# Kernel tuning notes

Measured on AMD Instinct MI355X. Metric: run time of the kernel, lower is better.

Reference implementation:

```python
import jax, jax.numpy as jnp
import numpy as np

N = 40000      # nodes
E = 320000     # edges (avg degree 8)
F_IN = 128     # input channels
H = 4          # attention heads
C = 64         # per-head hidden channels (hidden_features_size entries)
HC = H * C     # 256, width after head concat
OUT = 64       # output classes
BN_EPS = 1e-5
NEG_SLOPE = 0.2


def setup_inputs() -> dict:
    key = jax.random.key(0)
    ks = jax.random.split(key, 16)
    s1 = 1.0 / np.sqrt(F_IN)
    s2 = 1.0 / np.sqrt(HC)
    return {
        "x": jax.random.normal(ks[0], (N, F_IN), jnp.float32),
        "edge_index": jax.random.randint(ks[1], (2, E), 0, N, dtype=jnp.int64),
        "W1": jax.random.normal(ks[2], (F_IN, HC), jnp.float32) * s1,
        "a1_src": jax.random.normal(ks[3], (H, C), jnp.float32) * s2,
        "a1_dst": jax.random.normal(ks[4], (H, C), jnp.float32) * s2,
        "b1": jnp.zeros((HC,), jnp.float32),
        # BatchNorm1d(256)
        "bn1_gamma": jnp.ones((HC,), jnp.float32),
        "bn1_beta": jnp.zeros((HC,), jnp.float32),
        "W2": jax.random.normal(ks[5], (HC, HC), jnp.float32) * s2,
        "a2_src": jax.random.normal(ks[6], (H, C), jnp.float32) * s2,
        "a2_dst": jax.random.normal(ks[7], (H, C), jnp.float32) * s2,
        "b2": jnp.zeros((HC,), jnp.float32),
        # final projection Linear(256 -> 64)
        "linW": jax.random.normal(ks[8], (HC, OUT), jnp.float32) * s2,
        "linb": jnp.zeros((OUT,), jnp.float32),
    }


def gat_conv(x, W, a_src, a_dst, bias, src, dst):
    """PyG GATConv (concat=True, add_self_loops=False, negative_slope=0.2)."""
    h = (x @ W).reshape(-1, H, C)                       # [N,H,C]
    e_src = jnp.einsum("nhc,hc->nh", h, a_src)          # [N,H]
    e_dst = jnp.einsum("nhc,hc->nh", h, a_dst)          # [N,H]
    # per-edge unnormalized attention, message src -> dst
    e = jax.nn.leaky_relu(e_src[src] + e_dst[dst], NEG_SLOPE)   # [E,H]
    # segment softmax over incoming edges of each dst node
    m = jax.ops.segment_max(e, dst, num_segments=N)             # [N,H]
    p = jnp.exp(e - jax.lax.stop_gradient(m)[dst])              # [E,H]
    denom = jax.ops.segment_sum(p, dst, num_segments=N)         # [N,H]
    alpha = p / (denom[dst] + 1e-16)                            # [E,H]
    # weighted scatter-sum aggregation
    out = jax.ops.segment_sum(h[src] * alpha[:, :, None], dst, num_segments=N)  # [N,H,C]
    return out.reshape(-1, HC) + bias


def batch_norm(x, gamma, beta):
    mean = jnp.mean(x, axis=0)
    var = jnp.mean(jnp.square(x - mean), axis=0)
    return (x - mean) * jax.lax.rsqrt(var + BN_EPS) * gamma + beta


def reference(x, edge_index, W1, a1_src, a1_dst, b1, bn1_gamma, bn1_beta,
              W2, a2_src, a2_dst, b2, linW, linb):
    src, dst = edge_index[0], edge_index[1]
    h1 = gat_conv(x, W1, a1_src, a1_dst, b1, src, dst)
    h1 = jax.nn.elu(batch_norm(h1, bn1_gamma, bn1_beta))
    # dropout is identity in eval mode
    h2 = gat_conv(h1, W2, a2_src, a2_dst, b2, src, dst)
    # JumpingKnowledge 'max': elementwise max over layer outputs
    jk = jnp.maximum(h1, h2)
    return jk @ linW + linb
```

## Files before the change

kernel.cpp:

```cpp
#include <hip/hip_runtime.h>
#include <math.h>

#define N_NODES 40000
#define N_EDGES 320000
#define F_IN 128
#define NHEAD 4
#define HC 256
#define NOUT 64
#define SLOTCAP 40

typedef __attribute__((ext_vector_type(8))) __bf16 bf16x8;
typedef __attribute__((ext_vector_type(4))) float f32x4;

static __device__ __forceinline__ unsigned short f2bf(float f) {
    union { float f; unsigned u; } v; v.f = f;
    unsigned r = v.u + 0x7FFFu + ((v.u >> 16) & 1u);
    return (unsigned short)(r >> 16);
}
static __device__ __forceinline__ float bf2f(unsigned short s) {
    union { unsigned u; float f; } v; v.u = ((unsigned)s) << 16;
    return v.f;
}

__global__ __launch_bounds__(256) void prep_kernel(const float* __restrict__ W1,
                                                   const float* __restrict__ W2,
                                                   const float* __restrict__ linW,
                                                   unsigned short* __restrict__ W1t,
                                                   unsigned short* __restrict__ W2t,
                                                   unsigned short* __restrict__ linWt,
                                                   int* __restrict__ zero_ints,
                                                   float* __restrict__ bnacc) {
    int b = blockIdx.x, tid = threadIdx.x;
    if (b < 128) {
        int t = b * 256 + tid;
        int k = t >> 8, n = t & 255;
        W1t[n * 128 + k] = f2bf(W1[t]);
    } else if (b < 384) {
        int t = (b - 128) * 256 + tid;
        int k = t >> 8, n = t & 255;
        W2t[n * 256 + k] = f2bf(W2[t]);
    } else if (b < 448) {
        int t = (b - 384) * 256 + tid;
        int k = t >> 6, n = t & 63;
        linWt[n * 256 + k] = f2bf(linW[t]);
    } else if (b < 488) {
        int i = (b - 448) * 1024 + tid * 4;
        if (i < 40004) *(int4*)(zero_ints + i) = make_int4(0, 0, 0, 0);
    } else {
        if (tid < 512) bnacc[tid] = 0.f;
    }
}

template <int AMODE, int SCATTER>
__global__ __launch_bounds__(256) void gemm_wide(const void* __restrict__ Aptr,
                                                 const unsigned short* __restrict__ Bt,
                                                 const float* __restrict__ sc,
                                                 unsigned short* __restrict__ h1p,
                                                 unsigned short* __restrict__ Cb,
                                                 const float* __restrict__ asrc,
                                                 const float* __restrict__ adst,
                                                 float* __restrict__ es,
                                                 float* __restrict__ ed,
                                                 int K,
                                                 const int* __restrict__ ei,
                                                 int* __restrict__ cursor,
                                                 int* __restrict__ esorted) {
    __shared__ unsigned short As[64 * 32];
    __shared__ unsigned short Bs[256 * 32];
    int tid = threadIdx.x;
    if (SCATTER && blockIdx.x >= N_NODES / 64) {
        int e = (blockIdx.x - N_NODES / 64) * 256 + tid;
        if (e < N_EDGES) {
            int d = ei[N_EDGES + e];
            int s = ei[e];
            int pos = atomicAdd(&cursor[d], 1);
            esorted[d * SLOTCAP + pos] = s;
        }
        return;
    }
    int row0 = blockIdx.x * 64;
    int w = tid >> 6, lane = tid & 63;
    int quad = lane >> 4, l16 = lane & 15;
    f32x4 acc[4][4];
#pragma unroll
    for (int mi = 0; mi < 4; ++mi)
#pragma unroll
        for (int ni = 0; ni < 4; ++ni) acc[mi][ni] = (f32x4){0.f, 0.f, 0.f, 0.f};

    int srow = tid >> 2, schunk = (tid & 3) * 8;
    int brow = tid >> 1, bchunk = (tid & 1) * 16;

    float4 pa0, pa1;
    int4 pai;
    int4 pb[4];
    if (AMODE == 1) {
        const float* Af = (const float*)Aptr;
        size_t base = (size_t)(row0 + srow) * K + schunk;
        pa0 = *(const float4*)(Af + base);
        pa1 = *(const float4*)(Af + base + 4);
    } else {
        pai = *(const int4*)((const unsigned short*)Aptr + (size_t)(row0 + srow) * K + schunk);
    }
    {
        const unsigned short* s0 = Bt + (size_t)brow * K + bchunk;
        const unsigned short* s1 = Bt + (size_t)(128 + brow) * K + bchunk;
        pb[0] = *(const int4*)s0; pb[1] = *(const int4*)(s0 + 8);
        pb[2] = *(const int4*)s1; pb[3] = *(const int4*)(s1 + 8);
    }

    for (int kc = 0; kc < K; kc += 32) {
        union { int4 v; unsigned short u[8]; } aS;
        if (AMODE == 1) {
            aS.u[0] = f2bf(pa0.x); aS.u[1] = f2bf(pa0.y);
            aS.u[2] = f2bf(pa0.z); aS.u[3] = f2bf(pa0.w);
            aS.u[4] = f2bf(pa1.x); aS.u[5] = f2bf(pa1.y);
            aS.u[6] = f2bf(pa1.z); aS.u[7] = f2bf(pa1.w);
        } else {
            union { int4 v; unsigned short u[8]; } a;
            a.v = pai;
#pragma unroll
            for (int j = 0; j < 8; ++j) {
                int c = kc + schunk + j;
                float v = bf2f(a.u[j]) * sc[c] + sc[HC + c];
                v = v > 0.f ? v : (__expf(v) - 1.f);
                aS.u[j] = f2bf(v);
            }
        }
        int4 bS0 = pb[0], bS1 = pb[1], bS2 = pb[2], bS3 = pb[3];
        int kn = kc + 32;
        if (kn < K) {
            if (AMODE == 1) {
                const float* Af = (const float*)Aptr;
                size_t base = (size_t)(row0 + srow) * K + kn + schunk;
                pa0 = *(const float4*)(Af + base);
                pa1 = *(const float4*)(Af + base + 4);
            } else {
                pai = *(const int4*)((const unsigned short*)Aptr +
                                     (size_t)(row0 + srow) * K + kn + schunk);
            }
            const unsigned short* s0 = Bt + (size_t)brow * K + kn + bchunk;
            const unsigned short* s1 = Bt + (size_t)(128 + brow) * K + kn + bchunk;
            pb[0] = *(const int4*)s0; pb[1] = *(const int4*)(s0 + 8);
            pb[2] = *(const int4*)s1; pb[3] = *(const int4*)(s1 + 8);
        }
        *(int4*)(&As[srow * 32 + schunk]) = aS.v;
        if (AMODE == 3)
            *(int4*)(h1p + (size_t)(row0 + srow) * HC + kc + schunk) = aS.v;
        *(int4*)(&Bs[brow * 32 + bchunk]) = bS0;
        *(int4*)(&Bs[brow * 32 + bchunk + 8]) = bS1;
        *(int4*)(&Bs[(128 + brow) * 32 + bchunk]) = bS2;
        *(int4*)(&Bs[(128 + brow) * 32 + bchunk + 8]) = bS3;
        __syncthreads();
        bf16x8 af[4], bfr[4];
#pragma unroll
        for (int mi = 0; mi < 4; ++mi)
            af[mi] = *(const bf16x8*)(&As[(mi * 16 + l16) * 32 + quad * 8]);
#pragma unroll
        for (int ni = 0; ni < 4; ++ni)
            bfr[ni] = *(const bf16x8*)(&Bs[(w * 64 + ni * 16 + l16) * 32 + quad * 8]);
#pragma unroll
        for (int mi = 0; mi < 4; ++mi)
#pragma unroll
            for (int ni = 0; ni < 4; ++ni)
                acc[mi][ni] = __builtin_amdgcn_mfma_f32_16x16x32_bf16(
                    af[mi], bfr[ni], acc[mi][ni], 0, 0, 0);
        __syncthreads();
    }
#pragma unroll
    for (int mi = 0; mi < 4; ++mi)
#pragma unroll
        for (int ni = 0; ni < 4; ++ni) {
            int r0 = row0 + mi * 16 + quad * 4;
            int c = w * 64 + ni * 16 + l16;
#pragma unroll
            for (int r = 0; r < 4; ++r)
                Cb[(size_t)(r0 + r) * HC + c] = f2bf(acc[mi][ni][r]);
        }
    float as_v[4], ad_v[4];
#pragma unroll
    for (int ni = 0; ni < 4; ++ni) {
        int cl = ni * 16 + l16;
        as_v[ni] = asrc[w * 64 + cl];
        ad_v[ni] = adst[w * 64 + cl];
    }
#pragma unroll
    for (int mi = 0; mi < 4; ++mi)
#pragma unroll
        for (int r = 0; r < 4; ++r) {
            float s = 0.f, d = 0.f;
#pragma unroll
            for (int ni = 0; ni < 4; ++ni) {
                s += acc[mi][ni][r] * as_v[ni];
                d += acc[mi][ni][r] * ad_v[ni];
            }
#pragma unroll
            for (int off = 1; off < 16; off <<= 1) {
                s += __shfl_xor(s, off);
                d += __shfl_xor(d, off);
            }
            if (l16 == 0) {
                int row = row0 + mi * 16 + quad * 4 + r;
                es[(size_t)row * NHEAD + w] = s;
                ed[(size_t)row * NHEAD + w] = d;
            }
        }
}

__global__ __launch_bounds__(256) void final_gemm(const unsigned short* __restrict__ A,
                                                  const unsigned short* __restrict__ Bt,
                                                  const float* __restrict__ bias,
                                                  float* __restrict__ Cf) {
    __shared__ unsigned short As[64 * 32];
    __shared__ unsigned short Bs[64 * 32];
    int tid = threadIdx.x;
    int row0 = blockIdx.x * 64;
    int wave = tid >> 6, lane = tid & 63;
    int wm = wave >> 1, wn = wave & 1;
    int quad = lane >> 4, l16 = lane & 15;
    f32x4 acc[2][2];
#pragma unroll
    for (int mi = 0; mi < 2; ++mi)
#pragma unroll
        for (int ni = 0; ni < 2; ++ni) acc[mi][ni] = (f32x4){0.f, 0.f, 0.f, 0.f};

    int srow = tid >> 2, schunk = (tid & 3) * 8;
    int4 pa = *(const int4*)(A + (size_t)(row0 + srow) * HC + schunk);
    int4 pbv = *(const int4*)(Bt + (size_t)srow * HC + schunk);

    for (int kc = 0; kc < HC; kc += 32) {
        int4 aS = pa, bS = pbv;
        int kn = kc + 32;
        if (kn < HC) {
            pa = *(const int4*)(A + (size_t)(row0 + srow) * HC + kn + schunk);
            pbv = *(const int4*)(Bt + (size_t)srow * HC + kn + schunk);
        }
        *(int4*)(&As[srow * 32 + schunk]) = aS;
        *(int4*)(&Bs[srow * 32 + schunk]) = bS;
        __syncthreads();
        bf16x8 af[2], bfr[2];
#pragma unroll
        for (int mi = 0; mi < 2; ++mi)
            af[mi] = *(const bf16x8*)(&As[(wm * 32 + mi * 16 + l16) * 32 + quad * 8]);
#pragma unroll
        for (int ni = 0; ni < 2; ++ni)
            bfr[ni] = *(const bf16x8*)(&Bs[(wn * 32 + ni * 16 + l16) * 32 + quad * 8]);
#pragma unroll
        for (int mi = 0; mi < 2; ++mi)
#pragma unroll
            for (int ni = 0; ni < 2; ++ni)
                acc[mi][ni] = __builtin_amdgcn_mfma_f32_16x16x32_bf16(
                    af[mi], bfr[ni], acc[mi][ni], 0, 0, 0);
        __syncthreads();
    }
#pragma unroll
    for (int mi = 0; mi < 2; ++mi)
#pragma unroll
        for (int ni = 0; ni < 2; ++ni) {
            int r0 = row0 + wm * 32 + mi * 16 + quad * 4;
            int c = wn * 32 + ni * 16 + l16;
#pragma unroll
            for (int r = 0; r < 4; ++r)
                Cf[(size_t)(r0 + r) * NOUT + c] = acc[mi][ni][r] + bias[c];
        }
}

template <int JK>
__global__ __launch_bounds__(256) void aggregate_kernel(const unsigned short* __restrict__ h,
                                                        const float* __restrict__ es,
                                                        const float* __restrict__ ed,
                                                        const int* __restrict__ deg,
                                                        const int* __restrict__ esorted,
                                                        const float* __restrict__ bias,
                                                        const unsigned short* __restrict__ h1p,
                                                        unsigned short* __restrict__ outb) {
    int tid = threadIdx.x;
    int wave = tid >> 6, lane = tid & 63;
    int half = lane >> 5, l = lane & 31;
    int node = blockIdx.x * 8 + wave * 2 + half;
    int hh = l >> 3;
    float edv = ed[node * NHEAD + hh];
    int d = deg[node];
    int beg = node * SLOTCAP;
    float dsum = 0.f;
    float a[8] = {0.f, 0.f, 0.f, 0.f, 0.f, 0.f, 0.f, 0.f};
    for (int i = 0; i < d; i += 8) {
        int s[8];
        int4 hv[8];
        float ep[8];
#pragma unroll
        for (int j = 0; j < 8; ++j) {
            int slot = i + j;
            s[j] = esorted[beg + (slot < d ? slot : d - 1)];
        }
#pragma unroll
        for (int j = 0; j < 8; ++j)
            hv[j] = *(const int4*)(h + (size_t)s[j] * HC + l * 8);
#pragma unroll
        for (int j = 0; j < 8; ++j)
            ep[j] = es[s[j] * NHEAD + hh];
#pragma unroll
        for (int j = 0; j < 8; ++j) {
            float e = ep[j] + edv;
            e = e > 0.f ? e : 0.2f * e;
            float w = __expf(e);
            w = (i + j < d) ? w : 0.f;
            dsum += w;
            union { int4 v; unsigned short u[8]; } hu;
            hu.v = hv[j];
#pragma unroll
            for (int k = 0; k < 8; ++k) a[k] += w * bf2f(hu.u[k]);
        }
    }
    float inv = 1.f / (dsum + 1e-16f);
    float4 bv0 = *(const float4*)(bias + l * 8);
    float4 bv1 = *(const float4*)(bias + l * 8 + 4);
    float bb[8] = {bv0.x, bv0.y, bv0.z, bv0.w, bv1.x, bv1.y, bv1.z, bv1.w};
    union { int4 v; unsigned short u[8]; } o;
    if (JK == 0) {
#pragma unroll
        for (int k = 0; k < 8; ++k) o.u[k] = f2bf(a[k] * inv + bb[k]);
    } else {
        union { int4 v; unsigned short u[8]; } h1u;
        h1u.v = *(const int4*)(h1p + (size_t)node * HC + l * 8);
#pragma unroll
        for (int k = 0; k < 8; ++k)
            o.u[k] = f2bf(fmaxf(bf2f(h1u.u[k]), a[k] * inv + bb[k]));
    }
    *(int4*)(outb + (size_t)node * HC + l * 8) = o.v;
}

__global__ __launch_bounds__(256) void bn_stats_kernel(const unsigned short* __restrict__ x,
                                                       float* __restrict__ acc,
                                                       const float* __restrict__ gamma,
                                                       const float* __restrict__ beta,
                                                       float* __restrict__ sc,
                                                       int* __restrict__ ticket) {
    int c = threadIdx.x;
    int r0 = blockIdx.x * 200;
    float s = 0.f, s2 = 0.f;
    for (int r = r0; r < r0 + 200; ++r) {
        float v = bf2f(x[(size_t)r * HC + c]);
        s += v; s2 += v * v;
    }
    atomicAdd(&acc[c], s);
    atomicAdd(&acc[HC + c], s2);
    __threadfence();
    __syncthreads();
    __shared__ int is_last;
    if (c == 0) is_last = (atomicAdd(ticket, 1) == (int)gridDim.x - 1);
    __syncthreads();
    if (is_last) {
        float sum = atomicAdd(&acc[c], 0.f);
        float sq  = atomicAdd(&acc[HC + c], 0.f);
        float mean = sum * (1.f / N_NODES);
        float var = sq * (1.f / N_NODES) - mean * mean;
        float inv = rsqrtf(var + 1e-5f);
        float scale = gamma[c] * inv;
        sc[c] = scale;
        sc[HC + c] = beta[c] - mean * scale;
    }
}

extern "C" void kernel_launch(void* const* d_in, const int* in_sizes, int n_in,
                              void* d_out, int out_size, void* d_ws, size_t ws_size,
                              hipStream_t stream) {
    const float* x      = (const float*)d_in[0];
    const int*   ei     = (const int*)d_in[1];
    const float* W1     = (const float*)d_in[2];
    const float* a1_src = (const float*)d_in[3];
    const float* a1_dst = (const float*)d_in[4];
    const float* b1     = (const float*)d_in[5];
    const float* bn_g   = (const float*)d_in[6];
    const float* bn_b   = (const float*)d_in[7];
    const float* W2     = (const float*)d_in[8];
    const float* a2_src = (const float*)d_in[9];
    const float* a2_dst = (const float*)d_in[10];
    const float* b2     = (const float*)d_in[11];
    const float* linW   = (const float*)d_in[12];
    const float* linb   = (const float*)d_in[13];
    float* out = (float*)d_out;

    char* ws = (char*)d_ws;
    const size_t NHC_BF = (size_t)N_NODES * HC * 2;
    unsigned short* hpre_b  = (unsigned short*)(ws);
    unsigned short* h1agg_b = (unsigned short*)(ws + NHC_BF);
    unsigned short* h1p_b   = (unsigned short*)(ws + 2 * NHC_BF);
    unsigned short* jk_b    = (unsigned short*)(ws + 3 * NHC_BF);
    char* p = ws + 4 * NHC_BF;
    unsigned short* W1t   = (unsigned short*)p; p += (size_t)F_IN * HC * 2;
    unsigned short* W2t   = (unsigned short*)p; p += (size_t)HC * HC * 2;
    unsigned short* linWt = (unsigned short*)p; p += (size_t)HC * NOUT * 2;
    float* e_src   = (float*)p;  p += (size_t)N_NODES * NHEAD * 4;
    float* e_dst   = (float*)p;  p += (size_t)N_NODES * NHEAD * 4;
    int*   cursor  = (int*)p;    p += (size_t)N_NODES * 4;
    int*   ticket  = (int*)p;    p += 4 * 4;
    int*   esorted = (int*)p;    p += (size_t)N_NODES * SLOTCAP * 4;
    float* bnacc   = (float*)p;  p += 2 * HC * 4;
    float* bnsc    = (float*)p;  p += 2 * HC * 4;

    prep_kernel<<<489, 256, 0, stream>>>(W1, W2, linW, W1t, W2t, linWt, cursor, bnacc);

    gemm_wide<1, 1><<<N_NODES / 64 + (N_EDGES + 255) / 256, 256, 0, stream>>>(
        x, W1t, nullptr, nullptr, hpre_b, a1_src, a1_dst, e_src, e_dst, F_IN,
        ei, cursor, esorted);

    aggregate_kernel<0><<<N_NODES / 8, 256, 0, stream>>>(
        hpre_b, e_src, e_dst, cursor, esorted, b1, nullptr, h1agg_b);

    bn_stats_kernel<<<N_NODES / 200, 256, 0, stream>>>(h1agg_b, bnacc, bn_g, bn_b,
                                                       bnsc, ticket);

    gemm_wide<3, 0><<<N_NODES / 64, 256, 0, stream>>>(
        h1agg_b, W2t, bnsc, h1p_b, hpre_b, a2_src, a2_dst, e_src, e_dst, HC,
        nullptr, nullptr, nullptr);

    aggregate_kernel<1><<<N_NODES / 8, 256, 0, stream>>>(
        hpre_b, e_src, e_dst, cursor, esorted, b2, h1p_b, jk_b);

    final_gemm<<<N_NODES / 64, 256, 0, stream>>>(jk_b, linWt, linb, out);
}
```

Measured before the change: 241.4 us.

## Fuse layer-2 aggregation, JK max, and final linear projection into one kernel

After: 230.7 us. 1.05x faster.

```diff
diff --git a/kernel.cpp b/kernel.cpp
--- a/kernel.cpp
+++ b/kernel.cpp
@@ -206,64 +206,6 @@
         }
 }
 
-__global__ __launch_bounds__(256) void final_gemm(const unsigned short* __restrict__ A,
-                                                  const unsigned short* __restrict__ Bt,
-                                                  const float* __restrict__ bias,
-                                                  float* __restrict__ Cf) {
-    __shared__ unsigned short As[64 * 32];
-    __shared__ unsigned short Bs[64 * 32];
-    int tid = threadIdx.x;
-    int row0 = blockIdx.x * 64;
-    int wave = tid >> 6, lane = tid & 63;
-    int wm = wave >> 1, wn = wave & 1;
-    int quad = lane >> 4, l16 = lane & 15;
-    f32x4 acc[2][2];
-#pragma unroll
-    for (int mi = 0; mi < 2; ++mi)
-#pragma unroll
-        for (int ni = 0; ni < 2; ++ni) acc[mi][ni] = (f32x4){0.f, 0.f, 0.f, 0.f};
-
-    int srow = tid >> 2, schunk = (tid & 3) * 8;
-    int4 pa = *(const int4*)(A + (size_t)(row0 + srow) * HC + schunk);
-    int4 pbv = *(const int4*)(Bt + (size_t)srow * HC + schunk);
-
-    for (int kc = 0; kc < HC; kc += 32) {
-        int4 aS = pa, bS = pbv;
-        int kn = kc + 32;
-        if (kn < HC) {
-            pa = *(const int4*)(A + (size_t)(row0 + srow) * HC + kn + schunk);
-            pbv = *(const int4*)(Bt + (size_t)srow * HC + kn + schunk);
-        }
-        *(int4*)(&As[srow * 32 + schunk]) = aS;
-        *(int4*)(&Bs[srow * 32 + schunk]) = bS;
-        __syncthreads();
-        bf16x8 af[2], bfr[2];
-#pragma unroll
-        for (int mi = 0; mi < 2; ++mi)
-            af[mi] = *(const bf16x8*)(&As[(wm * 32 + mi * 16 + l16) * 32 + quad * 8]);
-#pragma unroll
-        for (int ni = 0; ni < 2; ++ni)
-            bfr[ni] = *(const bf16x8*)(&Bs[(wn * 32 + ni * 16 + l16) * 32 + quad * 8]);
-#pragma unroll
-        for (int mi = 0; mi < 2; ++mi)
-#pragma unroll
-            for (int ni = 0; ni < 2; ++ni)
-                acc[mi][ni] = __builtin_amdgcn_mfma_f32_16x16x32_bf16(
-                    af[mi], bfr[ni], acc[mi][ni], 0, 0, 0);
-        __syncthreads();
-    }
-#pragma unroll
-    for (int mi = 0; mi < 2; ++mi)
-#pragma unroll
-        for (int ni = 0; ni < 2; ++ni) {
-            int r0 = row0 + wm * 32 + mi * 16 + quad * 4;
-            int c = wn * 32 + ni * 16 + l16;
-#pragma unroll
-            for (int r = 0; r < 4; ++r)
-                Cf[(size_t)(r0 + r) * NOUT + c] = acc[mi][ni][r] + bias[c];
-        }
-}
-
 template <int JK>
 __global__ __launch_bounds__(256) void aggregate_kernel(const unsigned short* __restrict__ h,
                                                         const float* __restrict__ es,
@@ -329,6 +271,96 @@
     *(int4*)(outb + (size_t)node * HC + l * 8) = o.v;
 }
 
+__global__ __launch_bounds__(512) void aggregate2_fused(const unsigned short* __restrict__ h,
+                                                        const float* __restrict__ es,
+                                                        const float* __restrict__ ed,
+                                                        const int* __restrict__ deg,
+                                                        const int* __restrict__ esorted,
+                                                        const float* __restrict__ bias,
+                                                        const unsigned short* __restrict__ h1p,
+                                                        const unsigned short* __restrict__ linWt,
+                                                        const float* __restrict__ linb,
+                                                        float* __restrict__ out) {
+    __shared__ unsigned short jkS[16 * 264];
+    __shared__ unsigned short BsF[64 * 264];
+    int tid = threadIdx.x;
+    {
+        int n = tid >> 3, k0 = (tid & 7) * 32;
+        const int4* src = (const int4*)(linWt + n * 256 + k0);
+        int4 v0 = src[0], v1 = src[1], v2 = src[2], v3 = src[3];
+        int4* dstp = (int4*)(&BsF[n * 264 + k0]);
+        dstp[0] = v0; dstp[1] = v1; dstp[2] = v2; dstp[3] = v3;
+    }
+    int wave = tid >> 6, lane = tid & 63;
+    int half = lane >> 5, l = lane & 31;
+    int nloc = wave * 2 + half;
+    int node = blockIdx.x * 16 + nloc;
+    int hh = l >> 3;
+    float edv = ed[node * NHEAD + hh];
+    int d = deg[node];
+    int beg = node * SLOTCAP;
+    float dsum = 0.f;
+    float a[8] = {0.f, 0.f, 0.f, 0.f, 0.f, 0.f, 0.f, 0.f};
+    for (int i = 0; i < d; i += 8) {
+        int s[8];
+        int4 hv[8];
+        float ep[8];
+#pragma unroll
+        for (int j = 0; j < 8; ++j) {
+            int slot = i + j;
+            s[j] = esorted[beg + (slot < d ? slot : d - 1)];
+        }
+#pragma unroll
+        for (int j = 0; j < 8; ++j)
+            hv[j] = *(const int4*)(h + (size_t)s[j] * HC + l * 8);
+#pragma unroll
+        for (int j = 0; j < 8; ++j)
+            ep[j] = es[s[j] * NHEAD + hh];
+#pragma unroll
+        for (int j = 0; j < 8; ++j) {
+            float e = ep[j] + edv;
+            e = e > 0.f ? e : 0.2f * e;
+            float w = __expf(e);
+            w = (i + j < d) ? w : 0.f;
+            dsum += w;
+            union { int4 v; unsigned short u[8]; } hu;
+            hu.v = hv[j];
+#pragma unroll
+            for (int k = 0; k < 8; ++k) a[k] += w * bf2f(hu.u[k]);
+        }
+    }
+    float inv = 1.f / (dsum + 1e-16f);
+    float4 bv0 = *(const float4*)(bias + l * 8);
+    float4 bv1 = *(const float4*)(bias + l * 8 + 4);
+    float bb[8] = {bv0.x, bv0.y, bv0.z, bv0.w, bv1.x, bv1.y, bv1.z, bv1.w};
+    union { int4 v; unsigned short u[8]; } o;
+    {
+        union { int4 v; unsigned short u[8]; } h1u;
+        h1u.v = *(const int4*)(h1p + (size_t)node * HC + l * 8);
+#pragma unroll
+        for (int k = 0; k < 8; ++k)
+            o.u[k] = f2bf(fmaxf(bf2f(h1u.u[k]), a[k] * inv + bb[k]));
+    }
+    *(int4*)(&jkS[nloc * 264 + l * 8]) = o.v;
+    __syncthreads();
+    if (wave < 4) {
+        int quad = lane >> 4, l16 = lane & 15;
+        f32x4 acc = (f32x4){0.f, 0.f, 0.f, 0.f};
+#pragma unroll
+        for (int kc = 0; kc < HC; kc += 32) {
+            bf16x8 af = *(const bf16x8*)(&jkS[l16 * 264 + kc + quad * 8]);
+            bf16x8 bfr = *(const bf16x8*)(&BsF[(wave * 16 + l16) * 264 + kc + quad * 8]);
+            acc = __builtin_amdgcn_mfma_f32_16x16x32_bf16(af, bfr, acc, 0, 0, 0);
+        }
+        int row0 = blockIdx.x * 16 + quad * 4;
+        int c = wave * 16 + l16;
+        float bc = linb[c];
+#pragma unroll
+        for (int r = 0; r < 4; ++r)
+            out[(size_t)(row0 + r) * NOUT + c] = acc[r] + bc;
+    }
+}
+
 __global__ __launch_bounds__(256) void bn_stats_kernel(const unsigned short* __restrict__ x,
                                                        float* __restrict__ acc,
                                                        const float* __restrict__ gamma,
@@ -385,7 +417,6 @@
     unsigned short* hpre_b  = (unsigned short*)(ws);
     unsigned short* h1agg_b = (unsigned short*)(ws + NHC_BF);
     unsigned short* h1p_b   = (unsigned short*)(ws + 2 * NHC_BF);
-    unsigned short* jk_b    = (unsigned short*)(ws + 3 * NHC_BF);
     char* p = ws + 4 * NHC_BF;
     unsigned short* W1t   = (unsigned short*)p; p += (size_t)F_IN * HC * 2;
     unsigned short* W2t   = (unsigned short*)p; p += (size_t)HC * HC * 2;
@@ -414,8 +445,6 @@
         h1agg_b, W2t, bnsc, h1p_b, hpre_b, a2_src, a2_dst, e_src, e_dst, HC,
         nullptr, nullptr, nullptr);
 
-    aggregate_kernel<1><<<N_NODES / 8, 256, 0, stream>>>(
-        hpre_b, e_src, e_dst, cursor, esorted, b2, h1p_b, jk_b);
-
-    final_gemm<<<N_NODES / 64, 256, 0, stream>>>(jk_b, linWt, linb, out);
-}
+    aggregate2_fused<<<N_NODES / 16, 512, 0, stream>>>(
+        hpre_b, e_src, e_dst, cursor, esorted, b2, h1p_b, linWt, linb, out);
+}
```
